# Optimization experiments

Measured on AMD Instinct MI355X. Metric: run time of the kernel, lower is better.

The kernel has to match this reference:

```python
import jax, jax.numpy as jnp
import numpy as np

N_NODES = 50000
N_EDGES = 500000
D = 128
VOCAB = 10000
OUT = 64
LAYERS = 3
N_GRAPHS = 512


def setup_inputs() -> dict:
    key = jax.random.key(0)
    ks = jax.random.split(key, 10)
    nodes = jax.random.randint(ks[0], (N_NODES,), 0, VOCAB)
    edges = jax.random.randint(ks[1], (2, N_EDGES), 0, N_NODES)
    indices = jax.random.randint(ks[2], (N_NODES,), 0, N_GRAPHS)
    emb = jax.random.normal(ks[3], (VOCAB, D), dtype=jnp.float32) * 0.02
    W0 = jax.random.normal(ks[4], (LAYERS, D, D), dtype=jnp.float32) * (1.0 / np.sqrt(D))
    W1 = jax.random.normal(ks[5], (LAYERS, D, D), dtype=jnp.float32) * (1.0 / np.sqrt(D))
    W2 = jax.random.normal(ks[6], (LAYERS, D, D), dtype=jnp.float32) * (1.0 / np.sqrt(D))
    Wout = jax.random.normal(ks[7], (2 * D, OUT), dtype=jnp.float32) * (1.0 / np.sqrt(2 * D))
    bout = jnp.zeros((OUT,), dtype=jnp.float32)
    return {"nodes": nodes, "edges": edges, "indices": indices, "num_graphs": N_GRAPHS,
            "emb": emb, "W0": W0, "W1": W1, "W2": W2, "Wout": Wout, "bout": bout}


def reference(nodes, edges, indices, num_graphs, emb, W0, W1, W2, Wout, bout):
    n = nodes.shape[0]
    h = emb[nodes]  # [N, D]; Dropout(0.5) is identity in eval mode
    src, dst = edges[0], edges[1]
    seg = jnp.concatenate([dst, src])  # message destinations, [2E]
    deg = jax.ops.segment_sum(jnp.ones_like(seg, dtype=h.dtype), seg, num_segments=n)
    deg = jnp.maximum(deg, 1.0)[:, None]
    for l in range(W0.shape[0]):
        # per-edge linear on gathered endpoints (nn.Linear: x @ W.T)
        m = jnp.concatenate([h[src] @ W1[l].T, h[dst] @ W2[l].T], axis=0)  # [2E, D]
        msg = jax.ops.segment_sum(m, seg, num_segments=n) / deg  # scatter_mean
        h = jax.nn.relu(h @ W0[l].T + msg)
    # graph pooling: scatter_mean + scatter_max
    cnt = jax.ops.segment_sum(jnp.ones((n,), h.dtype), indices, num_segments=num_graphs)
    mean = jax.ops.segment_sum(h, indices, num_segments=num_graphs) / jnp.maximum(cnt, 1.0)[:, None]
    mx = jax.ops.segment_max(h, indices, num_segments=num_graphs)
    mx = jnp.where(jnp.isfinite(mx), mx, 0.0)  # empty segments -> 0 (torch_scatter default)
    v = jnp.concatenate([mean, mx], axis=1)  # [G, 2D]
    return v @ Wout + bout
```

## Files before the change

### kernel.cpp

```cpp
#include <hip/hip_runtime.h>
#include <hip/hip_bf16.h>

#define D 128
#define GRAPHS 512
#define OUTD 64
#define NC 8

typedef _Float16 half4v __attribute__((ext_vector_type(4)));
typedef _Float16 half8v __attribute__((ext_vector_type(8)));
typedef float float4v __attribute__((ext_vector_type(4)));
typedef float float8v __attribute__((ext_vector_type(8)));
typedef unsigned short u16;

__global__ void hist_kernel(const int* __restrict__ edges, const int* __restrict__ indices,
                            int* cnt_in8, int* cnt_out8, int* gcnt8,
                            u16* __restrict__ rank_in, u16* __restrict__ rank_out,
                            u16* __restrict__ grank,
                            const int* __restrict__ nodes, const float* __restrict__ emb,
                            _Float16* __restrict__ h,
                            const float* __restrict__ W0, const float* __restrict__ W1,
                            const float* __restrict__ W2, _Float16* __restrict__ Wpk,
                            int E, int n) {
    int i = blockIdx.x * 256 + threadIdx.x;
    int c = (i >> 8) & (NC - 1);
    if (i < E) {
        int s = edges[i];
        int d = edges[E + i];
        rank_out[i] = (u16)atomicAdd(&cnt_out8[c * n + s], 1);
        rank_in[i]  = (u16)atomicAdd(&cnt_in8[c * n + d], 1);
    }
    if (i < n) grank[i] = (u16)atomicAdd(&gcnt8[c * GRAPHS + indices[i]], 1);
    if (i < n * 16) {
        int v = i >> 4, q = i & 15;
        const float4* e4 = (const float4*)emb + (size_t)nodes[v] * 32 + q * 2;
        float4 f0 = e4[0];
        float4 f1 = e4[1];
        half8v o = {(_Float16)f0.x, (_Float16)f0.y, (_Float16)f0.z, (_Float16)f0.w,
                    (_Float16)f1.x, (_Float16)f1.y, (_Float16)f1.z, (_Float16)f1.w};
        ((half8v*)h)[i] = o;
    }
    if (i < 36864) {
        int j4 = (i & 1) * 4;
        int t = i >> 1;
        int lane = t & 63; t >>= 6;
        int nf = t & 7;   t >>= 3;
        int ks = t & 3;   t >>= 2;
        int src = t % 3;
        int l = t / 3;
        const float* W = (src == 0 ? W0 : (src == 1 ? W1 : W2)) + l * D * D;
        int col = nf * 16 + (lane & 15);
        int k = ks * 32 + (lane >> 4) * 8 + j4;
        float4 f = *(const float4*)&W[col * D + k];
        half4v o = {(_Float16)f.x, (_Float16)f.y, (_Float16)f.z, (_Float16)f.w};
        _Float16* dst = Wpk + ((size_t)(((l * 3 + src) * 4 + ks) * 8 + nf) * 64 + lane) * 8 + j4;
        *(half4v*)dst = o;
    }
}

__global__ __launch_bounds__(256) void offsets_kernel(
    const int* __restrict__ cnt_in8, int* __restrict__ o8_in, int* __restrict__ off_in,
    int* __restrict__ tot_in,
    const int* __restrict__ cnt_out8, int* __restrict__ o8_out, int* __restrict__ off_out,
    int* __restrict__ tot_out,
    const int* __restrict__ gcnt8, int* __restrict__ o8_g, int* __restrict__ goff,
    int* __restrict__ gtot,
    int* totals, int n) {
    __shared__ int ws[8];
    int tid = threadIdx.x;
    int lane = tid & 63, wid = tid >> 6;
    int i = blockIdx.x * 256 + tid;

#define SCAN8(cnt8, o8, off, tot_arr, total, len)                          \
    do {                                                                   \
        int c8_[NC]; int tot_ = 0;                                         \
        if (i < (len)) {                                                   \
            _Pragma("unroll") for (int k_ = 0; k_ < NC; ++k_) {            \
                c8_[k_] = (cnt8)[k_ * (len) + i]; tot_ += c8_[k_];         \
            }                                                              \
        }                                                                  \
        int v_ = tot_;                                                     \
        _Pragma("unroll") for (int d_ = 1; d_ < 64; d_ <<= 1) {            \
            int t_ = __shfl_up(v_, d_, 64);                                \
            if (lane >= d_) v_ += t_;                                      \
        }                                                                  \
        if (lane == 63) ws[wid] = v_;                                      \
        __syncthreads();                                                   \
        if (tid == 0) {                                                    \
            int s_ = 0;                                                    \
            for (int k_ = 0; k_ < 4; ++k_) { int t_ = ws[k_]; ws[k_] = s_; s_ += t_; } \
            ws[4] = atomicAdd((total), s_);                                \
        }                                                                  \
        __syncthreads();                                                   \
        if (i < (len)) {                                                   \
            int run_ = ws[4] + ws[wid] + v_ - tot_;                        \
            (off)[i] = run_; (tot_arr)[i] = tot_;                          \
            _Pragma("unroll") for (int k_ = 0; k_ < NC; ++k_) {            \
                (o8)[k_ * (len) + i] = run_; run_ += c8_[k_];              \
            }                                                              \
        }                                                                  \
        __syncthreads();                                                   \
    } while (0)

    SCAN8(cnt_in8, o8_in, off_in, tot_in, &totals[0], n);
    SCAN8(cnt_out8, o8_out, off_out, tot_out, &totals[1], n);
    if (blockIdx.x < 2) SCAN8(gcnt8, o8_g, goff, gtot, &totals[2], GRAPHS);
#undef SCAN8
}

__global__ void fill_kernel(const int* __restrict__ edges, const int* __restrict__ indices,
                            const int* __restrict__ o8_in, const int* __restrict__ o8_out,
                            const int* __restrict__ o8_g,
                            const u16* __restrict__ rank_in, const u16* __restrict__ rank_out,
                            const u16* __restrict__ grank,
                            u16* __restrict__ csr_in, u16* __restrict__ csr_out,
                            u16* __restrict__ glist, int E, int n) {
    int i = blockIdx.x * 256 + threadIdx.x;
    int c = (i >> 8) & (NC - 1);
    if (i < E) {
        int s = edges[i];
        int d = edges[E + i];
        csr_in[o8_in[c * n + d] + rank_in[i]]   = (u16)s;
        csr_out[o8_out[c * n + s] + rank_out[i]] = (u16)d;
    }
    if (i < n)
        glist[o8_g[c * GRAPHS + indices[i]] + grank[i]] = (u16)i;
}

__global__ __launch_bounds__(256) void aggregate_kernel(
    const _Float16* __restrict__ h,
    const u16* __restrict__ csr_in, const int* __restrict__ off_in, const int* __restrict__ cnt_in,
    const u16* __restrict__ csr_out, const int* __restrict__ off_out, const int* __restrict__ cnt_out,
    _Float16* __restrict__ agg1, _Float16* __restrict__ agg2, int n) {
    int grp = threadIdx.x >> 4;
    int lane = threadIdx.x & 15;
    int v = blockIdx.x * 16 + grp;
    if (v >= n) return;
    int s1 = off_in[v], c1 = cnt_in[v];
    int s2 = off_out[v], c2 = cnt_out[v];
    float invd = 1.0f / fmaxf((float)(c1 + c2), 1.0f);
    const half8v* h8 = (const half8v*)h;

    float8v a1 = {0.f, 0.f, 0.f, 0.f, 0.f, 0.f, 0.f, 0.f};
    int i = 0;
    for (; i + 4 <= c1; i += 4) {
        int u0 = csr_in[s1 + i], u1 = csr_in[s1 + i + 1];
        int u2 = csr_in[s1 + i + 2], u3 = csr_in[s1 + i + 3];
        half8v p0 = h8[u0 * 16 + lane];
        half8v p1 = h8[u1 * 16 + lane];
        half8v p2 = h8[u2 * 16 + lane];
        half8v p3 = h8[u3 * 16 + lane];
        a1 += (__builtin_convertvector(p0, float8v) + __builtin_convertvector(p1, float8v)) +
              (__builtin_convertvector(p2, float8v) + __builtin_convertvector(p3, float8v));
    }
    for (; i < c1; ++i)
        a1 += __builtin_convertvector(h8[csr_in[s1 + i] * 16 + lane], float8v);

    float8v a2 = {0.f, 0.f, 0.f, 0.f, 0.f, 0.f, 0.f, 0.f};
    i = 0;
    for (; i + 4 <= c2; i += 4) {
        int u0 = csr_out[s2 + i], u1 = csr_out[s2 + i + 1];
        int u2 = csr_out[s2 + i + 2], u3 = csr_out[s2 + i + 3];
        half8v p0 = h8[u0 * 16 + lane];
        half8v p1 = h8[u1 * 16 + lane];
        half8v p2 = h8[u2 * 16 + lane];
        half8v p3 = h8[u3 * 16 + lane];
        a2 += (__builtin_convertvector(p0, float8v) + __builtin_convertvector(p1, float8v)) +
              (__builtin_convertvector(p2, float8v) + __builtin_convertvector(p3, float8v));
    }
    for (; i < c2; ++i)
        a2 += __builtin_convertvector(h8[csr_out[s2 + i] * 16 + lane], float8v);

    a1 *= invd;
    a2 *= invd;
    ((half8v*)agg1)[v * 16 + lane] = __builtin_convertvector(a1, half8v);
    ((half8v*)agg2)[v * 16 + lane] = __builtin_convertvector(a2, half8v);
}

__global__ __launch_bounds__(128) void transform_mfma(
    const _Float16* __restrict__ Xh, const _Float16* __restrict__ A1,
    const _Float16* __restrict__ A2, const _Float16* __restrict__ Wl,
    _Float16* __restrict__ Hout, int n) {
    __shared__ _Float16 Hs[64][136];
    int tid = threadIdx.x;
    int w = tid >> 6, lane = tid & 63;
    int rbase = blockIdx.x * 64 + w * 32;
    int m0 = lane & 15;
    int kg = lane >> 4;
    int r0 = min(rbase + m0, n - 1);
    int r1 = min(rbase + 16 + m0, n - 1);

    const _Float16* srcs[3] = {Xh, A1, A2};

    float4v acc[2][8];
#pragma unroll
    for (int mf = 0; mf < 2; ++mf)
#pragma unroll
        for (int nf = 0; nf < 8; ++nf) acc[mf][nf] = (float4v){0.f, 0.f, 0.f, 0.f};

#define LOAD_STEP(stp, A0v, A1v, Bv)                                              \
    do {                                                                          \
        const int src_ = (stp) >> 2, ks_ = (stp) & 3;                             \
        const _Float16* X_ = srcs[src_];                                          \
        A0v = *(const half8v*)(X_ + (size_t)r0 * D + ks_ * 32 + kg * 8);          \
        A1v = *(const half8v*)(X_ + (size_t)r1 * D + ks_ * 32 + kg * 8);          \
        const _Float16* wp_ = Wl + (size_t)((src_ * 4 + ks_) * 8) * 512 + lane * 8; \
        _Pragma("unroll") for (int nf_ = 0; nf_ < 8; ++nf_)                       \
            Bv[nf_] = *(const half8v*)(wp_ + nf_ * 512);                          \
    } while (0)

    half8v a0c, a1c, bc[8], a0n, a1n, bn[8];
    LOAD_STEP(0, a0c, a1c, bc);
#pragma unroll
    for (int step = 0; step < 12; ++step) {
        if (step < 11) LOAD_STEP(step + 1, a0n, a1n, bn);
#pragma unroll
        for (int nf = 0; nf < 8; ++nf) {
            acc[0][nf] = __builtin_amdgcn_mfma_f32_16x16x32_f16(a0c, bc[nf], acc[0][nf], 0, 0, 0);
            acc[1][nf] = __builtin_amdgcn_mfma_f32_16x16x32_f16(a1c, bc[nf], acc[1][nf], 0, 0, 0);
        }
        a0c = a0n; a1c = a1n;
#pragma unroll
        for (int nf = 0; nf < 8; ++nf) bc[nf] = bn[nf];
    }
#undef LOAD_STEP

#pragma unroll
    for (int mf = 0; mf < 2; ++mf)
#pragma unroll
        for (int nf = 0; nf < 8; ++nf)
#pragma unroll
            for (int r = 0; r < 4; ++r) {
                int row = w * 32 + mf * 16 + kg * 4 + r;
                int col = nf * 16 + m0;
                Hs[row][col] = (_Float16)fmaxf(acc[mf][nf][r], 0.0f);
            }
    __syncthreads();
#pragma unroll
    for (int it = 0; it < 8; ++it) {
        int id = tid + it * 128;
        int row = id >> 4, c8 = id & 15;
        int grow = blockIdx.x * 64 + row;
        if (grow < n)
            *(half8v*)(Hout + (size_t)grow * D + c8 * 8) = *(const half8v*)&Hs[row][c8 * 8];
    }
}

__global__ __launch_bounds__(128) void pool_head_kernel(
    const _Float16* __restrict__ h, const u16* __restrict__ glist,
    const int* __restrict__ goff, const int* __restrict__ gcnt,
    const float* __restrict__ Wout, const float* __restrict__ bout,
    float* __restrict__ out) {
    __shared__ float feat[2 * D];
    int g = blockIdx.x;
    int t = threadIdx.x;
    int s = goff[g], c = gcnt[g];
    float sum = 0.0f, mx = 0.0f;
    int i = 0;
    for (; i + 4 <= c; i += 4) {
        int v0 = glist[s + i], v1 = glist[s + i + 1];
        int v2 = glist[s + i + 2], v3 = glist[s + i + 3];
        float a = (float)h[(size_t)v0 * D + t];
        float b = (float)h[(size_t)v1 * D + t];
        float cc = (float)h[(size_t)v2 * D + t];
        float d = (float)h[(size_t)v3 * D + t];
        sum += (a + b) + (cc + d);
        mx = fmaxf(mx, fmaxf(fmaxf(a, b), fmaxf(cc, d)));
    }
    for (; i < c; ++i) {
        float a = (float)h[(size_t)glist[s + i] * D + t];
        sum += a;
        mx = fmaxf(mx, a);
    }
    feat[t] = sum / fmaxf((float)c, 1.0f);
    feat[D + t] = mx;
    __syncthreads();
    if (t < OUTD) {
        float acc = bout[t];
#pragma unroll 8
        for (int k = 0; k < 2 * D; ++k)
            acc = fmaf(feat[k], Wout[k * OUTD + t], acc);
        out[g * OUTD + t] = acc;
    }
}

extern "C" void kernel_launch(void* const* d_in, const int* in_sizes, int n_in,
                              void* d_out, int out_size, void* d_ws, size_t ws_size,
                              hipStream_t stream) {
    const int* nodes   = (const int*)d_in[0];
    const int* edges   = (const int*)d_in[1];
    const int* indices = (const int*)d_in[2];
    const float* emb  = (const float*)d_in[4];
    const float* W0   = (const float*)d_in[5];
    const float* W1   = (const float*)d_in[6];
    const float* W2   = (const float*)d_in[7];
    const float* Wout = (const float*)d_in[8];
    const float* bout = (const float*)d_in[9];
    float* out = (float*)d_out;

    const int n = in_sizes[0];
    const int E = in_sizes[1] / 2;

    char* ws = (char*)d_ws;
    size_t off = 0;
    auto alloc = [&](size_t bytes) -> char* {
        char* p = ws + off;
        off = (off + bytes + 255) & ~(size_t)255;
        return p;
    };
    int* cnt_in8  = (int*)alloc((size_t)NC * n * sizeof(int));
    int* cnt_out8 = (int*)alloc((size_t)NC * n * sizeof(int));
    int* gcnt8    = (int*)alloc(NC * GRAPHS * sizeof(int));
    int* totals   = (int*)alloc(3 * sizeof(int));
    size_t zbytes = off;
    int* o8_in   = (int*)alloc((size_t)NC * n * sizeof(int));
    int* o8_out  = (int*)alloc((size_t)NC * n * sizeof(int));
    int* o8_g    = (int*)alloc(NC * GRAPHS * sizeof(int));
    int* off_in  = (int*)alloc(n * sizeof(int));
    int* off_out = (int*)alloc(n * sizeof(int));
    int* tot_in  = (int*)alloc(n * sizeof(int));
    int* tot_out = (int*)alloc(n * sizeof(int));
    int* goff    = (int*)alloc(GRAPHS * sizeof(int));
    int* gtot    = (int*)alloc(GRAPHS * sizeof(int));
    u16* rank_in  = (u16*)alloc(E * sizeof(u16));
    u16* rank_out = (u16*)alloc(E * sizeof(u16));
    u16* grank    = (u16*)alloc(n * sizeof(u16));
    u16* glist   = (u16*)alloc(n * sizeof(u16));
    u16* csr_in  = (u16*)alloc(E * sizeof(u16));
    u16* csr_out = (u16*)alloc(E * sizeof(u16));
    _Float16* Wpk = (_Float16*)alloc(3 * 3 * 4 * 8 * 64 * 8 * sizeof(_Float16));
    _Float16* B0 = (_Float16*)alloc((size_t)n * D * sizeof(_Float16));
    _Float16* B1 = (_Float16*)alloc((size_t)n * D * sizeof(_Float16));
    _Float16* B2 = (_Float16*)alloc((size_t)n * D * sizeof(_Float16));
    (void)ws_size;

    hipMemsetAsync(d_ws, 0, zbytes, stream);

    int hblocks = (n * 16 + 255) / 256;
    hist_kernel<<<hblocks, 256, 0, stream>>>(edges, indices, cnt_in8, cnt_out8, gcnt8,
                                             rank_in, rank_out, grank,
                                             nodes, emb, B0, W0, W1, W2, Wpk, E, n);
    int oblocks = (n + 255) / 256;
    offsets_kernel<<<oblocks, 256, 0, stream>>>(cnt_in8, o8_in, off_in, tot_in,
                                                cnt_out8, o8_out, off_out, tot_out,
                                                gcnt8, o8_g, goff, gtot, totals, n);
    int eblocks = (E + 255) / 256;
    fill_kernel<<<eblocks, 256, 0, stream>>>(edges, indices, o8_in, o8_out, o8_g,
                                             rank_in, rank_out, grank,
                                             csr_in, csr_out, glist, E, n);

    int ablocks = (n + 15) / 16;
    int tblocks = (n + 63) / 64;
    for (int l = 0; l < 3; ++l) {
        aggregate_kernel<<<ablocks, 256, 0, stream>>>(B0, csr_in, off_in, tot_in,
                                                      csr_out, off_out, tot_out, B1, B2, n);
        transform_mfma<<<tblocks, 128, 0, stream>>>(B0, B1, B2,
                                                    Wpk + (size_t)l * 3 * 4 * 8 * 512,
                                                    B0, n);
    }

    pool_head_kernel<<<GRAPHS, 128, 0, stream>>>(B0, glist, goff, gtot, Wout, bout, out);
}
```

Measured before the change: 316.1 us.

## Build CSR with LDS-privatized histograms over node ranges and edge slices

Replaces global-atomic histogramming with stored ranks by a 64-range x 16-slice block grid. Each block counts its own node range in shared memory with LDS atomics, then refills positions the same way, so no per-edge rank arrays or global atomics are needed. The cost is that every block rescans its whole edge slice, reading the edge array 64 times across ranges. Ordering inside a bucket becomes nondeterministic, but sums are unaffected.

```diff
diff --git a/kernel.cpp b/kernel.cpp
--- a/kernel.cpp
+++ b/kernel.cpp
@@ -4,7 +4,10 @@
 #define D 128
 #define GRAPHS 512
 #define OUTD 64
-#define NC 8
+#define NR 64
+#define NSL 16
+#define NSCAN (NR * NSL)
+#define LRANGE 800
 
 typedef _Float16 half4v __attribute__((ext_vector_type(4)));
 typedef _Float16 half8v __attribute__((ext_vector_type(8)));
@@ -12,24 +15,70 @@
 typedef float float8v __attribute__((ext_vector_type(8)));
 typedef unsigned short u16;
 
-__global__ void hist_kernel(const int* __restrict__ edges, const int* __restrict__ indices,
-                            int* cnt_in8, int* cnt_out8, int* gcnt8,
-                            u16* __restrict__ rank_in, u16* __restrict__ rank_out,
-                            u16* __restrict__ grank,
-                            const int* __restrict__ nodes, const float* __restrict__ emb,
-                            _Float16* __restrict__ h,
-                            const float* __restrict__ W0, const float* __restrict__ W1,
-                            const float* __restrict__ W2, _Float16* __restrict__ Wpk,
-                            int E, int n) {
-    int i = blockIdx.x * 256 + threadIdx.x;
-    int c = (i >> 8) & (NC - 1);
-    if (i < E) {
-        int s = edges[i];
-        int d = edges[E + i];
-        rank_out[i] = (u16)atomicAdd(&cnt_out8[c * n + s], 1);
-        rank_in[i]  = (u16)atomicAdd(&cnt_in8[c * n + d], 1);
-    }
-    if (i < n) grank[i] = (u16)atomicAdd(&gcnt8[c * GRAPHS + indices[i]], 1);
+__global__ __launch_bounds__(256) void prep_kernel(
+    const int* __restrict__ edges, const int* __restrict__ indices,
+    int* __restrict__ pc_in, int* __restrict__ pc_out, int* __restrict__ pc_g,
+    const int* __restrict__ nodes, const float* __restrict__ emb,
+    _Float16* __restrict__ h,
+    const float* __restrict__ W0, const float* __restrict__ W1,
+    const float* __restrict__ W2, _Float16* __restrict__ Wpk,
+    int E, int n) {
+    int tid = threadIdx.x;
+    if (blockIdx.x < NSCAN) {
+        __shared__ int lin[LRANGE];
+        __shared__ int lout[LRANGE];
+        int s = blockIdx.x >> 6;
+        int r = blockIdx.x & (NR - 1);
+        int range = (n + NR - 1) / NR;
+        int lo = r * range, hi = min(lo + range, n), len = hi - lo;
+        for (int j = tid; j < len; j += 256) { lin[j] = 0; lout[j] = 0; }
+        __syncthreads();
+        int echunk = (((E + NSL - 1) / NSL) + 3) & ~3;
+        int elo = s * echunk, ehi = min(elo + echunk, E);
+#define HI(arr, k) { unsigned r_ = (unsigned)((k) - lo); if (r_ < (unsigned)len) atomicAdd(&arr[r_], 1); }
+        {
+            const int4* s4 = (const int4*)(edges + elo);
+            const int4* d4 = (const int4*)(edges + E + elo);
+            int m4 = (ehi - elo) >> 2;
+            for (int it = tid; it < m4; it += 256) {
+                int4 sv = s4[it], dv = d4[it];
+                HI(lin, dv.x) HI(lin, dv.y) HI(lin, dv.z) HI(lin, dv.w)
+                HI(lout, sv.x) HI(lout, sv.y) HI(lout, sv.z) HI(lout, sv.w)
+            }
+            for (int e = elo + m4 * 4 + tid; e < ehi; e += 256) {
+                HI(lin, edges[E + e])
+                HI(lout, edges[e])
+            }
+        }
+#undef HI
+        __syncthreads();
+        for (int j = tid; j < len; j += 256) {
+            pc_in[s * n + lo + j] = lin[j];
+            pc_out[s * n + lo + j] = lout[j];
+        }
+        int grange = (GRAPHS + NR - 1) / NR;
+        int glo = r * grange, ghi = min(glo + grange, GRAPHS), glen = ghi - glo;
+        __syncthreads();
+        for (int j = tid; j < glen; j += 256) lin[j] = 0;
+        __syncthreads();
+        int ichunk = (((n + NSL - 1) / NSL) + 3) & ~3;
+        int ilo = s * ichunk, ihi = min(ilo + ichunk, n);
+#define GH(k) { unsigned r_ = (unsigned)((k) - glo); if (r_ < (unsigned)glen) atomicAdd(&lin[r_], 1); }
+        {
+            const int4* i4 = (const int4*)(indices + ilo);
+            int g4 = (ihi - ilo) >> 2;
+            for (int it = tid; it < g4; it += 256) {
+                int4 v = i4[it];
+                GH(v.x) GH(v.y) GH(v.z) GH(v.w)
+            }
+            for (int e = ilo + g4 * 4 + tid; e < ihi; e += 256) GH(indices[e])
+        }
+#undef GH
+        __syncthreads();
+        for (int j = tid; j < glen; j += 256) pc_g[s * GRAPHS + glo + j] = lin[j];
+        return;
+    }
+    int i = (blockIdx.x - NSCAN) * 256 + tid;
     if (i < n * 16) {
         int v = i >> 4, q = i & 15;
         const float4* e4 = (const float4*)emb + (size_t)nodes[v] * 32 + q * 2;
@@ -58,24 +107,24 @@
 }
 
 __global__ __launch_bounds__(256) void offsets_kernel(
-    const int* __restrict__ cnt_in8, int* __restrict__ o8_in, int* __restrict__ off_in,
-    int* __restrict__ tot_in,
-    const int* __restrict__ cnt_out8, int* __restrict__ o8_out, int* __restrict__ off_out,
-    int* __restrict__ tot_out,
-    const int* __restrict__ gcnt8, int* __restrict__ o8_g, int* __restrict__ goff,
-    int* __restrict__ gtot,
+    const int* __restrict__ pc_in, int* __restrict__ o16_in,
+    int* __restrict__ off_in, int* __restrict__ tot_in,
+    const int* __restrict__ pc_out, int* __restrict__ o16_out,
+    int* __restrict__ off_out, int* __restrict__ tot_out,
+    const int* __restrict__ pc_g, int* __restrict__ o16_g,
+    int* __restrict__ goff, int* __restrict__ gtot,
     int* totals, int n) {
     __shared__ int ws[8];
     int tid = threadIdx.x;
     int lane = tid & 63, wid = tid >> 6;
     int i = blockIdx.x * 256 + tid;
 
-#define SCAN8(cnt8, o8, off, tot_arr, total, len)                          \
+#define SCAN16(pc, o16, off, tot_arr, total, len)                          \
     do {                                                                   \
-        int c8_[NC]; int tot_ = 0;                                         \
+        int part_[NSL]; int tot_ = 0;                                      \
         if (i < (len)) {                                                   \
-            _Pragma("unroll") for (int k_ = 0; k_ < NC; ++k_) {            \
-                c8_[k_] = (cnt8)[k_ * (len) + i]; tot_ += c8_[k_];         \
+            _Pragma("unroll") for (int k_ = 0; k_ < NSL; ++k_) {           \
+                part_[k_] = (pc)[k_ * (len) + i]; tot_ += part_[k_];       \
             }                                                              \
         }                                                                  \
         int v_ = tot_;                                                     \
@@ -94,36 +143,81 @@
         if (i < (len)) {                                                   \
             int run_ = ws[4] + ws[wid] + v_ - tot_;                        \
             (off)[i] = run_; (tot_arr)[i] = tot_;                          \
-            _Pragma("unroll") for (int k_ = 0; k_ < NC; ++k_) {            \
-                (o8)[k_ * (len) + i] = run_; run_ += c8_[k_];              \
+            _Pragma("unroll") for (int k_ = 0; k_ < NSL; ++k_) {           \
+                (o16)[k_ * (len) + i] = run_; run_ += part_[k_];           \
             }                                                              \
         }                                                                  \
         __syncthreads();                                                   \
     } while (0)
 
-    SCAN8(cnt_in8, o8_in, off_in, tot_in, &totals[0], n);
-    SCAN8(cnt_out8, o8_out, off_out, tot_out, &totals[1], n);
-    if (blockIdx.x < 2) SCAN8(gcnt8, o8_g, goff, gtot, &totals[2], GRAPHS);
-#undef SCAN8
-}
-
-__global__ void fill_kernel(const int* __restrict__ edges, const int* __restrict__ indices,
-                            const int* __restrict__ o8_in, const int* __restrict__ o8_out,
-                            const int* __restrict__ o8_g,
-                            const u16* __restrict__ rank_in, const u16* __restrict__ rank_out,
-                            const u16* __restrict__ grank,
-                            u16* __restrict__ csr_in, u16* __restrict__ csr_out,
-                            u16* __restrict__ glist, int E, int n) {
-    int i = blockIdx.x * 256 + threadIdx.x;
-    int c = (i >> 8) & (NC - 1);
-    if (i < E) {
-        int s = edges[i];
-        int d = edges[E + i];
-        csr_in[o8_in[c * n + d] + rank_in[i]]   = (u16)s;
-        csr_out[o8_out[c * n + s] + rank_out[i]] = (u16)d;
-    }
-    if (i < n)
-        glist[o8_g[c * GRAPHS + indices[i]] + grank[i]] = (u16)i;
+    SCAN16(pc_in, o16_in, off_in, tot_in, &totals[0], n);
+    SCAN16(pc_out, o16_out, off_out, tot_out, &totals[1], n);
+    if (blockIdx.x < (GRAPHS + 255) / 256)
+        SCAN16(pc_g, o16_g, goff, gtot, &totals[2], GRAPHS);
+#undef SCAN16
+}
+
+__global__ __launch_bounds__(256) void fill_kernel(
+    const int* __restrict__ edges, const int* __restrict__ indices,
+    const int* __restrict__ o16_in, const int* __restrict__ o16_out,
+    const int* __restrict__ o16_g,
+    u16* __restrict__ csr_in, u16* __restrict__ csr_out, u16* __restrict__ glist,
+    int E, int n) {
+    __shared__ int cin[LRANGE];
+    __shared__ int cout[LRANGE];
+    __shared__ int cg[8];
+    int tid = threadIdx.x;
+    int s = blockIdx.x >> 6;
+    int r = blockIdx.x & (NR - 1);
+    int range = (n + NR - 1) / NR;
+    int lo = r * range, hi = min(lo + range, n), len = hi - lo;
+    int grange = (GRAPHS + NR - 1) / NR;
+    int glo = r * grange, ghi = min(glo + grange, GRAPHS), glen = ghi - glo;
+    for (int j = tid; j < len; j += 256) {
+        cin[j] = o16_in[s * n + lo + j];
+        cout[j] = o16_out[s * n + lo + j];
+    }
+    for (int j = tid; j < glen; j += 256) cg[j] = o16_g[s * GRAPHS + glo + j];
+    __syncthreads();
+
+    int echunk = (((E + NSL - 1) / NSL) + 3) & ~3;
+    int elo = s * echunk, ehi = min(elo + echunk, E);
+#define FIN(k, pay) { unsigned r_ = (unsigned)((k) - lo); if (r_ < (unsigned)len) { \
+        int p_ = atomicAdd(&cin[r_], 1); csr_in[p_] = (u16)(pay); } }
+#define FOUT(k, pay) { unsigned r_ = (unsigned)((k) - lo); if (r_ < (unsigned)len) { \
+        int p_ = atomicAdd(&cout[r_], 1); csr_out[p_] = (u16)(pay); } }
+    {
+        const int4* s4 = (const int4*)(edges + elo);
+        const int4* d4 = (const int4*)(edges + E + elo);
+        int m4 = (ehi - elo) >> 2;
+        for (int it = tid; it < m4; it += 256) {
+            int4 sv = s4[it], dv = d4[it];
+            FIN(dv.x, sv.x) FIN(dv.y, sv.y) FIN(dv.z, sv.z) FIN(dv.w, sv.w)
+            FOUT(sv.x, dv.x) FOUT(sv.y, dv.y) FOUT(sv.z, dv.z) FOUT(sv.w, dv.w)
+        }
+        for (int e = elo + m4 * 4 + tid; e < ehi; e += 256) {
+            int se = edges[e], de = edges[E + e];
+            FIN(de, se)
+            FOUT(se, de)
+        }
+    }
+#undef FIN
+#undef FOUT
+#define FG(g, vv) { unsigned r_ = (unsigned)((g) - glo); if (r_ < (unsigned)glen) { \
+        int p_ = atomicAdd(&cg[r_], 1); glist[p_] = (u16)(vv); } }
+    {
+        int ichunk = (((n + NSL - 1) / NSL) + 3) & ~3;
+        int ilo = s * ichunk, ihi = min(ilo + ichunk, n);
+        const int4* i4 = (const int4*)(indices + ilo);
+        int g4 = (ihi - ilo) >> 2;
+        for (int it = tid; it < g4; it += 256) {
+            int4 v = i4[it];
+            int e = ilo + it * 4;
+            FG(v.x, e) FG(v.y, e + 1) FG(v.z, e + 2) FG(v.w, e + 3)
+        }
+        for (int e = ilo + g4 * 4 + tid; e < ihi; e += 256) FG(indices[e], e)
+    }
+#undef FG
 }
 
 __global__ __launch_bounds__(256) void aggregate_kernel(
@@ -307,23 +401,20 @@
         off = (off + bytes + 255) & ~(size_t)255;
         return p;
     };
-    int* cnt_in8  = (int*)alloc((size_t)NC * n * sizeof(int));
-    int* cnt_out8 = (int*)alloc((size_t)NC * n * sizeof(int));
-    int* gcnt8    = (int*)alloc(NC * GRAPHS * sizeof(int));
-    int* totals   = (int*)alloc(3 * sizeof(int));
+    int* totals = (int*)alloc(3 * sizeof(int));
     size_t zbytes = off;
-    int* o8_in   = (int*)alloc((size_t)NC * n * sizeof(int));
-    int* o8_out  = (int*)alloc((size_t)NC * n * sizeof(int));
-    int* o8_g    = (int*)alloc(NC * GRAPHS * sizeof(int));
+    int* pc_in   = (int*)alloc((size_t)NSL * n * sizeof(int));
+    int* pc_out  = (int*)alloc((size_t)NSL * n * sizeof(int));
+    int* pc_g    = (int*)alloc(NSL * GRAPHS * sizeof(int));
+    int* o16_in  = (int*)alloc((size_t)NSL * n * sizeof(int));
+    int* o16_out = (int*)alloc((size_t)NSL * n * sizeof(int));
+    int* o16_g   = (int*)alloc(NSL * GRAPHS * sizeof(int));
     int* off_in  = (int*)alloc(n * sizeof(int));
     int* off_out = (int*)alloc(n * sizeof(int));
     int* tot_in  = (int*)alloc(n * sizeof(int));
     int* tot_out = (int*)alloc(n * sizeof(int));
     int* goff    = (int*)alloc(GRAPHS * sizeof(int));
     int* gtot    = (int*)alloc(GRAPHS * sizeof(int));
-    u16* rank_in  = (u16*)alloc(E * sizeof(u16));
-    u16* rank_out = (u16*)alloc(E * sizeof(u16));
-    u16* grank    = (u16*)alloc(n * sizeof(u16));
     u16* glist   = (u16*)alloc(n * sizeof(u16));
     u16* csr_in  = (u16*)alloc(E * sizeof(u16));
     u16* csr_out = (u16*)alloc(E * sizeof(u16));
@@ -335,18 +426,15 @@
 
     hipMemsetAsync(d_ws, 0, zbytes, stream);
 
-    int hblocks = (n * 16 + 255) / 256;
-    hist_kernel<<<hblocks, 256, 0, stream>>>(edges, indices, cnt_in8, cnt_out8, gcnt8,
-                                             rank_in, rank_out, grank,
+    int pblocks = NSCAN + (n * 16 + 255) / 256;
+    prep_kernel<<<pblocks, 256, 0, stream>>>(edges, indices, pc_in, pc_out, pc_g,
                                              nodes, emb, B0, W0, W1, W2, Wpk, E, n);
     int oblocks = (n + 255) / 256;
-    offsets_kernel<<<oblocks, 256, 0, stream>>>(cnt_in8, o8_in, off_in, tot_in,
-                                                cnt_out8, o8_out, off_out, tot_out,
-                                                gcnt8, o8_g, goff, gtot, totals, n);
-    int eblocks = (E + 255) / 256;
-    fill_kernel<<<eblocks, 256, 0, stream>>>(edges, indices, o8_in, o8_out, o8_g,
-                                             rank_in, rank_out, grank,
-                                             csr_in, csr_out, glist, E, n);
+    offsets_kernel<<<oblocks, 256, 0, stream>>>(pc_in, o16_in, off_in, tot_in,
+                                                pc_out, o16_out, off_out, tot_out,
+                                                pc_g, o16_g, goff, gtot, totals, n);
+    fill_kernel<<<NSCAN, 256, 0, stream>>>(edges, indices, o16_in, o16_out, o16_g,
+                                           csr_in, csr_out, glist, E, n);
 
     int ablocks = (n + 15) / 16;
     int tblocks = (n + 63) / 64;
```

After: 315.0 us, median of 3. No clear change (-0.4%).
